# Kernel tuning notes

Measured on AMD Instinct MI355X. Metric: run time of the kernel, lower is better.

Reference implementation:

```python
import jax, jax.numpy as jnp
import numpy as np

DIM = 256
N_CHANNELS = 8
NEIGHBORS = 16


def setup_inputs() -> dict:
    key = jax.random.key(0)
    kx, kw = jax.random.split(key)
    B, N, D = 4, 1024, DIM
    x = jax.random.normal(kx, (B, N, D), dtype=jnp.float32)
    # nn.Linear(dim, dim*2*n_channels, bias=False); store as [in, out] so y = x @ W
    W_qk = jax.random.normal(kw, (D, 2 * N_CHANNELS * D), dtype=jnp.float32) * (D ** -0.5)
    return {"x": x, "W_qk": W_qk}


def _norm_edge(edge):
    # edge: [B, C, N, N]
    norm_row = edge / (edge.sum(axis=-1, keepdims=True) + 1e-6)
    norm_col = norm_row / (norm_row.sum(axis=-2, keepdims=True) + 1e-6)
    # norm_row @ norm_col^T
    return jnp.einsum('bcnk,bcmk->bcnm', norm_row, norm_col)


def reference(x, W_qk):
    B, N, D = x.shape
    C = N_CHANNELS
    scale = D ** -0.5
    qk = (x @ W_qk).reshape(B, N, 2, C, D)
    q = jnp.transpose(qk[:, :, 0], (0, 2, 1, 3))  # [B, C, N, D]
    k = jnp.transpose(qk[:, :, 1], (0, 2, 1, 3))  # [B, C, N, D]
    attn = jax.nn.softmax(jnp.einsum('bcnd,bcmd->bcnm', q, k) * scale, axis=-1)

    # clip(): top-k neighbor mask from channel-summed (detached) attention
    sum_edge = jax.lax.stop_gradient(attn).sum(axis=1)  # [B, N, N]
    kk = min(NEIGHBORS, N)
    _, top_idx = jax.lax.top_k(sum_edge, kk)  # [B, N, kk]
    b_idx = jnp.arange(B)[:, None, None]
    r_idx = jnp.arange(N)[None, :, None]
    mask = jnp.zeros((B, N, N), dtype=attn.dtype).at[b_idx, r_idx, top_idx].set(1.0)
    mask = jnp.maximum(mask, jnp.eye(N, dtype=attn.dtype))  # identity diag
    edge = mask[:, None] * attn  # [B, C, N, N]
    return _norm_edge(edge)
```

## Files before the change

kernel.cpp:

```cpp
#include <hip/hip_runtime.h>
#include <hip/hip_bf16.h>
#include <math.h>

#define BB 4
#define NN 1024
#define DD 256
#define CC 8
#define KNBR 16
#define MAXSEL 17
#define ZCAP (NN * MAXSEL)

typedef _Float16 f16x8_t __attribute__((ext_vector_type(8)));
typedef _Float16 f16x4_t __attribute__((ext_vector_type(4)));
typedef float    f32x4_t __attribute__((ext_vector_type(4)));

__device__ __forceinline__ void gl2lds16(const _Float16* g, _Float16* ldsbase) {
    __builtin_amdgcn_global_load_lds(
        (const __attribute__((address_space(1))) unsigned int*)g,
        (__attribute__((address_space(3))) unsigned int*)ldsbase, 16, 0, 0);
}

__device__ __forceinline__ void split2(float v, _Float16& h, _Float16& l) {
    h = (_Float16)v;
    l = (_Float16)(v - (float)h);
}

__global__ __launch_bounds__(256) void split_all(const float* __restrict__ x,
                                                 const float* __restrict__ W,
                                                 _Float16* __restrict__ xh,
                                                 _Float16* __restrict__ xl,
                                                 _Float16* __restrict__ Wth,
                                                 _Float16* __restrict__ Wtl,
                                                 int* __restrict__ countb) {
    const int tid = threadIdx.x;
    if (blockIdx.x < 1024) {
        int i = (blockIdx.x * 256 + tid) * 4;
        float4 v = *(const float4*)(x + i);
        f16x4_t hv, lv;
        _Float16 h, l;
        split2(v.x, h, l); hv[0] = h; lv[0] = l;
        split2(v.y, h, l); hv[1] = h; lv[1] = l;
        split2(v.z, h, l); hv[2] = h; lv[2] = l;
        split2(v.w, h, l); hv[3] = h; lv[3] = l;
        *(f16x4_t*)(xh + i) = hv;
        *(f16x4_t*)(xl + i) = lv;
    } else {
        const int b2 = blockIdx.x - 1024;
        if (b2 == 0) {
            int4 zz = make_int4(0, 0, 0, 0);
#pragma unroll
            for (int g = 0; g < 4; g++) ((int4*)countb)[tid + 256 * g] = zz;
        }
        __shared__ float t[64][65];
        const int n0 = (b2 & 63) * 64;
        const int k0 = (b2 >> 6) * 64;
#pragma unroll
        for (int i = 0; i < 16; i++) {
            int k = i * 4 + (tid >> 6);
            int n = tid & 63;
            t[k][n] = W[(size_t)(k0 + k) * 4096 + n0 + n];
        }
        __syncthreads();
#pragma unroll
        for (int i = 0; i < 16; i++) {
            int n = i * 4 + (tid >> 6);
            int k = tid & 63;
            _Float16 h, l;
            split2(t[k][n] * 16.f, h, l);
            size_t o = (size_t)(n0 + n) * 256 + k0 + k;
            Wth[o] = h; Wtl[o] = l;
        }
    }
}

#define STG(dst, src, rowbase, kk)                                             \
    do {                                                                       \
        gl2lds16((src) + (size_t)((rowbase) + r_st) * 256 + (kk) + c8,         \
                 &(dst)[(w * 64) * 8]);                                        \
        gl2lds16((src) + (size_t)((rowbase) + 64 + r_st) * 256 + (kk) + c8,    \
                 &(dst)[(256 + w * 64) * 8]);                                  \
    } while (0)

#define MFMA3(accv, AH, AL, BH, BL)                                            \
    do {                                                                       \
        accv = __builtin_amdgcn_mfma_f32_16x16x32_f16(AL, BH, accv, 0, 0, 0);  \
        accv = __builtin_amdgcn_mfma_f32_16x16x32_f16(AH, BL, accv, 0, 0, 0);  \
        accv = __builtin_amdgcn_mfma_f32_16x16x32_f16(AH, BH, accv, 0, 0, 0);  \
    } while (0)

#define COMPUTE(AH, AL, BH, BL)                                                \
    do {                                                                       \
        f16x8_t ah[4], al[4];                                                  \
        _Pragma("unroll")                                                      \
        for (int mi = 0; mi < 4; mi++) {                                       \
            int r = (wr * 64 + mi * 16 + lm) * 32 + qx8;                       \
            ah[mi] = *(const f16x8_t*)&(AH)[r];                                \
            al[mi] = *(const f16x8_t*)&(AL)[r];                                \
        }                                                                      \
        _Pragma("unroll")                                                      \
        for (int ni = 0; ni < 4; ni++) {                                       \
            int rb = (wc * 64 + ni * 16 + lm) * 32 + qx8;                      \
            f16x8_t bh = *(const f16x8_t*)&(BH)[rb];                           \
            f16x8_t bl = *(const f16x8_t*)&(BL)[rb];                           \
            _Pragma("unroll")                                                  \
            for (int mi = 0; mi < 4; mi++)                                     \
                MFMA3(acc[mi][ni], ah[mi], al[mi], bh, bl);                    \
        }                                                                      \
    } while (0)

__global__ __launch_bounds__(256) void gemm_xw_mfma(
        const _Float16* __restrict__ xh, const _Float16* __restrict__ xl,
        const _Float16* __restrict__ wth, const _Float16* __restrict__ wtl,
        _Float16* __restrict__ qh, _Float16* __restrict__ ql,
        _Float16* __restrict__ kh, _Float16* __restrict__ kl) {
    __shared__ __align__(16) char smem[65536];
    _Float16* Ah0 = (_Float16*)smem;
    _Float16* Al0 = (_Float16*)(smem + 8192);
    _Float16* Bh0 = (_Float16*)(smem + 16384);
    _Float16* Bl0 = (_Float16*)(smem + 24576);
    _Float16* Ah1 = (_Float16*)(smem + 32768);
    _Float16* Al1 = (_Float16*)(smem + 40960);
    _Float16* Bh1 = (_Float16*)(smem + 49152);
    _Float16* Bl1 = (_Float16*)(smem + 57344);
    const int tid = threadIdx.x, lane = tid & 63, w = tid >> 6;
    const int wr = w >> 1, wc = w & 1;
    const int lm = lane & 15, quad = lane >> 4;
    const int row0 = blockIdx.y * 128, col0 = blockIdx.x * 128;
    const int r_st = tid >> 2;
    const int c8 = (((tid & 3) ^ ((tid >> 3) & 3)) * 8);
    const int qx8 = ((quad ^ ((lm >> 1) & 3)) * 8);

    f32x4_t acc[4][4];
#pragma unroll
    for (int i = 0; i < 4; i++)
#pragma unroll
        for (int j = 0; j < 4; j++) acc[i][j] = (f32x4_t)(0.f);

    STG(Ah0, xh, row0, 0); STG(Al0, xl, row0, 0);
    STG(Bh0, wth, col0, 0); STG(Bl0, wtl, col0, 0);
    __syncthreads();
#pragma unroll
    for (int t = 0; t < 8; t += 2) {
        {
            int kn = (t + 1) * 32;
            if (t + 1 < 8) {
                STG(Ah1, xh, row0, kn); STG(Al1, xl, row0, kn);
                STG(Bh1, wth, col0, kn); STG(Bl1, wtl, col0, kn);
            }
            COMPUTE(Ah0, Al0, Bh0, Bl0);
            __syncthreads();
        }
        {
            int kn = (t + 2) * 32;
            if (t + 2 < 8) {
                STG(Ah0, xh, row0, kn); STG(Al0, xl, row0, kn);
                STG(Bh0, wth, col0, kn); STG(Bl0, wtl, col0, kn);
            }
            COMPUTE(Ah1, Al1, Bh1, Bl1);
            __syncthreads();
        }
    }

    float* tr = (float*)smem;
    const int s = col0 >> 11, c = (col0 >> 8) & 7, dbase = col0 & 255;
    _Float16* dh = s ? kh : qh;
    _Float16* dl = s ? kl : ql;
    const int rl = tid >> 2;
    const int cb = (tid & 3) * 8;
#pragma unroll
    for (int p = 0; p < 2; p++) {
        if (p) __syncthreads();
        if (wr == p) {
#pragma unroll
            for (int mi = 0; mi < 4; mi++) {
                int rloc = mi * 16 + quad * 4;
#pragma unroll
                for (int ni = 0; ni < 4; ni++) {
                    int cl = wc * 64 + ni * 16 + lm;
#pragma unroll
                    for (int r = 0; r < 4; r++)
                        tr[(rloc + r) * 132 + cl] = acc[mi][ni][r];
                }
            }
        }
        __syncthreads();
        int rr = row0 + p * 64 + rl;
        int bb = rr >> 10, n = rr & 1023;
        size_t base = (((size_t)(bb * CC + c)) * NN + n) * DD + dbase;
#pragma unroll
        for (int g = 0; g < 4; g++) {
            int ccol = g * 32 + cb;
            f16x8_t hv, lv;
#pragma unroll
            for (int e = 0; e < 8; e++) {
                float vv = tr[rl * 132 + ccol + e];
                _Float16 h, l;
                split2(vv, h, l);
                hv[e] = h; lv[e] = l;
            }
            *(f16x8_t*)(dh + base + ccol) = hv;
            *(f16x8_t*)(dl + base + ccol) = lv;
        }
    }
}

__global__ __launch_bounds__(256) void gemm_qkt_mfma(
        const _Float16* __restrict__ qh, const _Float16* __restrict__ ql,
        const _Float16* __restrict__ kh, const _Float16* __restrict__ kl,
        float* __restrict__ attn) {
    __shared__ __align__(16) char smem[65536];
    _Float16* Ah0 = (_Float16*)smem;
    _Float16* Al0 = (_Float16*)(smem + 8192);
    _Float16* Bh0 = (_Float16*)(smem + 16384);
    _Float16* Bl0 = (_Float16*)(smem + 24576);
    _Float16* Ah1 = (_Float16*)(smem + 32768);
    _Float16* Al1 = (_Float16*)(smem + 40960);
    _Float16* Bh1 = (_Float16*)(smem + 49152);
    _Float16* Bl1 = (_Float16*)(smem + 57344);
    const int tid = threadIdx.x, lane = tid & 63, w = tid >> 6;
    const int wr = w >> 1, wc = w & 1;
    const int lm = lane & 15, quad = lane >> 4;
    const int id = blockIdx.x;
    const int rb8 = id & 7, qq = id >> 3;
    const int j = qq & 63, zhi = qq >> 6;
    const int z = zhi * 8 + rb8;
    const int row0 = (j >> 3) * 128, col0 = (j & 7) * 128;
    const size_t zo = (size_t)z * NN * DD;
    float* Cm = attn + (size_t)z * NN * NN;
    const int r_st = tid >> 2;
    const int c8 = (((tid & 3) ^ ((tid >> 3) & 3)) * 8);
    const int qx8 = ((quad ^ ((lm >> 1) & 3)) * 8);
    const float scale = 0.0625f / 256.0f;

    f32x4_t acc[4][4];
#pragma unroll
    for (int i = 0; i < 4; i++)
#pragma unroll
        for (int j2 = 0; j2 < 4; j2++) acc[i][j2] = (f32x4_t)(0.f);

    const _Float16* qhz = qh + zo;
    const _Float16* qlz = ql + zo;
    const _Float16* khz = kh + zo;
    const _Float16* klz = kl + zo;

    STG(Ah0, qhz, row0, 0); STG(Al0, qlz, row0, 0);
    STG(Bh0, khz, col0, 0); STG(Bl0, klz, col0, 0);
    __syncthreads();
#pragma unroll
    for (int t = 0; t < 8; t += 2) {
        {
            int kn = (t + 1) * 32;
            if (t + 1 < 8) {
                STG(Ah1, qhz, row0, kn); STG(Al1, qlz, row0, kn);
                STG(Bh1, khz, col0, kn); STG(Bl1, klz, col0, kn);
            }
            COMPUTE(Ah0, Al0, Bh0, Bl0);
            __syncthreads();
        }
        {
            int kn = (t + 2) * 32;
            if (t + 2 < 8) {
                STG(Ah0, qhz, row0, kn); STG(Al0, qlz, row0, kn);
                STG(Bh0, khz, col0, kn); STG(Bl0, klz, col0, kn);
            }
            COMPUTE(Ah1, Al1, Bh1, Bl1);
            __syncthreads();
        }
    }

#pragma unroll
    for (int mi = 0; mi < 4; mi++)
#pragma unroll
        for (int ni = 0; ni < 4; ni++) {
            int row = row0 + wr * 64 + mi * 16 + quad * 4;
            int col = col0 + wc * 64 + ni * 16 + lm;
#pragma unroll
            for (int r = 0; r < 4; r++)
                Cm[(size_t)(row + r) * NN + col] = acc[mi][ni][r] * scale;
        }
}

__global__ __launch_bounds__(256) void softmax_topk(const float* __restrict__ attn,
                                                    float2* __restrict__ ml,
                                                    int* __restrict__ idx,
                                                    int* __restrict__ cnt,
                                                    int* __restrict__ countb,
                                                    float* __restrict__ colsum) {
    __shared__ float psum[4][1280];
    __shared__ int fsel[MAXSEL];
    __shared__ int fcnt;
    const int bn = blockIdx.x, b = bn >> 10, n = bn & 1023;
    const int tid = threadIdx.x, lane = tid & 63, w = tid >> 6;

    if (tid < CC) colsum[(size_t)(b * CC + tid) * NN + n] = 0.f;

    const int colb = lane * 16;
    const int pb   = lane * 20;
    float4 u[2][4];
#pragma unroll
    for (int p = 0; p < 2; p++) {
        const int c = w * 2 + p;
        const float* rowp = attn + (((size_t)(b * CC + c) * NN + n) * NN) + colb;
#pragma unroll
        for (int g = 0; g < 4; g++) u[p][g] = *(const float4*)(rowp + g * 4);
    }

    float acc[16];
#pragma unroll
    for (int e = 0; e < 16; e++) acc[e] = 0.f;

#pragma unroll
    for (int p = 0; p < 2; p++) {
        const int c = w * 2 + p;
        const float* f = (const float*)&u[p][0];
        float mx = f[0];
#pragma unroll
        for (int e = 1; e < 16; e++) mx = fmaxf(mx, f[e]);
#pragma unroll
        for (int off = 1; off < 64; off <<= 1) mx = fmaxf(mx, __shfl_xor(mx, off));
        float sm = 0.f;
        float pe[16];
#pragma unroll
        for (int e = 0; e < 16; e++) { pe[e] = expf(f[e] - mx); sm += pe[e]; }
#pragma unroll
        for (int off = 1; off < 64; off <<= 1) sm += __shfl_xor(sm, off);
        if (lane == 0) ml[(size_t)(b * CC + c) * NN + n] = make_float2(mx, sm);
        float inv = 1.0f / sm;
#pragma unroll
        for (int e = 0; e < 16; e++) acc[e] += pe[e] * inv;
    }
#pragma unroll
    for (int g = 0; g < 4; g++)
        *(float4*)&psum[w][pb + g * 4] =
            make_float4(acc[g * 4], acc[g * 4 + 1], acc[g * 4 + 2], acc[g * 4 + 3]);
    __syncthreads();

    const int p4 = tid * 4 + (tid >> 2) * 4;
    float4 a0 = *(const float4*)&psum[0][p4];
    float4 a1 = *(const float4*)&psum[1][p4];
    float4 a2 = *(const float4*)&psum[2][p4];
    float4 a3 = *(const float4*)&psum[3][p4];
    float4 vs;
    vs.x = a0.x + a1.x + a2.x + a3.x;
    vs.y = a0.y + a1.y + a2.y + a3.y;
    vs.z = a0.z + a1.z + a2.z + a3.z;
    vs.w = a0.w + a1.w + a2.w + a3.w;
    *(float4*)&psum[0][p4] = vs;
    __syncthreads();

    if (w == 0) {
        unsigned vb[16];
#pragma unroll
        for (int g = 0; g < 4; g++) {
            float4 t4 = *(const float4*)&psum[0][pb + g * 4];
            vb[g * 4 + 0] = __float_as_uint(t4.x);
            vb[g * 4 + 1] = __float_as_uint(t4.y);
            vb[g * 4 + 2] = __float_as_uint(t4.z);
            vb[g * 4 + 3] = __float_as_uint(t4.w);
        }
        unsigned lo = 0u, hi = 0x7F800000u;
        while (lo < hi) {
            unsigned mid = lo + ((hi - lo) >> 1);
            int c = 0;
#pragma unroll
            for (int e = 0; e < 16; e++)
                c += (int)__popcll(__ballot(vb[e] > mid));
            if (c <= 15) hi = mid; else lo = mid + 1;
        }
        const unsigned V = hi;
        int cgt = 0, ceq = 0;
#pragma unroll
        for (int e = 0; e < 16; e++) {
            cgt += (vb[e] > V) ? 1 : 0;
            ceq += (vb[e] == V) ? 1 : 0;
        }
        int pk = cgt | (ceq << 16);
        int incl = pk;
#pragma unroll
        for (int o = 1; o < 64; o <<= 1) {
            int v2 = __shfl_up(incl, o);
            if (lane >= o) incl += v2;
        }
        int tot = __shfl(incl, 63);
        int c1 = tot & 0xffff;
        int need = KNBR - c1;
        int excl = incl - pk;
        int pg = excl & 0xffff;
        int pe2 = excl >> 16;
        int lg = 0, le = 0;
#pragma unroll
        for (int e = 0; e < 16; e++) {
            if (vb[e] > V) {
                fsel[pg + lg] = colb + e; lg++;
            } else if (vb[e] == V) {
                if (pe2 + le < need) fsel[c1 + pe2 + le] = colb + e;
                le++;
            }
        }
        if (lane == 0) {
            bool has = false;
#pragma unroll
            for (int t2 = 0; t2 < KNBR; t2++)
                if (fsel[t2] == n) has = true;
            int c = KNBR;
            if (!has) { fsel[KNBR] = n; c = KNBR + 1; }
            fcnt = c;
            cnt[bn] = c;
        }
    }
    __syncthreads();
    if (tid < fcnt) {
        idx[bn * MAXSEL + tid] = fsel[tid];
        atomicAdd(&countb[b * NN + fsel[tid]], 1);
    }
}

__global__ __launch_bounds__(256) void scan_offb(const int* __restrict__ countb,
                                                 int* __restrict__ offb,
                                                 int* __restrict__ curs) {
    __shared__ int wtot[4];
    const int b = blockIdx.x, tid = threadIdx.x, lane = tid & 63, w = tid >> 6;
    int c0 = countb[b * NN + tid * 4 + 0];
    int c1 = countb[b * NN + tid * 4 + 1];
    int c2 = countb[b * NN + tid * 4 + 2];
    int c3 = countb[b * NN + tid * 4 + 3];
    int tsum = c0 + c1 + c2 + c3;
    int incl = tsum;
#pragma unroll
    for (int off = 1; off < 64; off <<= 1) {
        int v = __shfl_up(incl, off);
        if (lane >= off) incl += v;
    }
    if (lane == 63) wtot[w] = incl;
    __syncthreads();
    int woff = 0;
    for (int i = 0; i < w; i++) woff += wtot[i];
    int base = woff + incl - tsum;
    int o0 = base, o1 = base + c0, o2 = base + c0 + c1, o3 = base + c0 + c1 + c2;
    offb[b * NN + tid * 4 + 0] = o0;
    offb[b * NN + tid * 4 + 1] = o1;
    offb[b * NN + tid * 4 + 2] = o2;
    offb[b * NN + tid * 4 + 3] = o3;
#pragma unroll
    for (int c = 0; c < CC; c++) {
        int z = b * CC + c;
        curs[z * NN + tid * 4 + 0] = o0;
        curs[z * NN + tid * 4 + 1] = o1;
        curs[z * NN + tid * 4 + 2] = o2;
        curs[z * NN + tid * 4 + 3] = o3;
    }
}

__global__ __launch_bounds__(256) void rownorm_fill(const float* __restrict__ attn,
                                                    const float2* __restrict__ ml,
                                                    const int* __restrict__ idx,
                                                    const int* __restrict__ cnt,
                                                    int* __restrict__ curs,
                                                    float* __restrict__ nr,
                                                    float* __restrict__ colsum,
                                                    int2* __restrict__ epack) {
    const int t = blockIdx.x * 256 + threadIdx.x;
    const int z = t >> 10, n = t & 1023;
    const int b = z >> 3;
    const int bn = b * NN + n;
    const int c_ = cnt[bn];
    const float* arow = attn + (size_t)t * NN;
    const float2 MM = ml[t];
    const float invl = 1.0f / MM.y;
    const size_t zb = (size_t)z * ZCAP;
    float a[MAXSEL];
    int kk[MAXSEL];
    float s = 0.f;
#pragma unroll
    for (int j = 0; j < MAXSEL; j++) {
        if (j < c_) {
            kk[j] = idx[bn * MAXSEL + j];
            float p = expf(arow[kk[j]] - MM.x) * invl;
            a[j] = p; s += p;
        }
    }
    const float inv = 1.f / (s + 1e-6f);
#pragma unroll
    for (int j = 0; j < MAXSEL; j++) {
        if (j < c_) {
            float v = a[j] * inv;
            nr[(size_t)t * MAXSEL + j] = v;
            atomicAdd(&colsum[(size_t)z * NN + kk[j]], v);
            int p = atomicAdd(&curs[z * NN + kk[j]], 1);
            epack[zb + p] = make_int2(n, __float_as_int(v));
        }
    }
}

__global__ __launch_bounds__(256) void out_sparse(const float* __restrict__ nr,
                                                  const int* __restrict__ idx,
                                                  const int* __restrict__ cnt,
                                                  const int* __restrict__ offb,
                                                  const int* __restrict__ countb,
                                                  const float* __restrict__ colsum,
                                                  const int2* __restrict__ epack,
                                                  float* __restrict__ out) {
    __shared__ float row[4][NN];
    const int tid = threadIdx.x, lane = tid & 63, w = tid >> 6;
    const int t = blockIdx.x * 4 + w;
    const int z = t >> 10;
    const int b = z >> 3;
    const int bn = b * NN + (t & 1023);
    const size_t zb = (size_t)z * ZCAP;

    f32x4_t zz = (f32x4_t)(0.f);
#pragma unroll
    for (int q = 0; q < 4; q++) ((f32x4_t*)row[w])[q * 64 + lane] = zz;

    const int c_ = cnt[bn];
    float sc = 0.f;
    int off = 0, len = 0;
    if (lane < c_) {
        int k = idx[bn * MAXSEL + lane];
        float wgt = nr[(size_t)t * MAXSEL + lane];
        sc = wgt / (colsum[(size_t)z * NN + k] + 1e-6f);
        off = offb[b * NN + k];
        len = countb[b * NN + k];
    }

    const int half = lane >> 5, l0 = lane & 31;
    for (int j = half; j < c_; j += 2) {
        float scj = __shfl(sc, j);
        int offj = __shfl(off, j);
        int lenj = __shfl(len, j);
        for (int l = l0; l < lenj; l += 32) {
            int2 ev = epack[zb + offj + l];
            atomicAdd(&row[w][ev.x], scj * __int_as_float(ev.y));
        }
    }
    const size_t ob = (size_t)t * NN;
    f32x4_t* op = (f32x4_t*)(out + ob);
#pragma unroll
    for (int q = 0; q < 4; q++)
        op[q * 64 + lane] = ((f32x4_t*)row[w])[q * 64 + lane];
}

extern "C" void kernel_launch(void* const* d_in, const int* in_sizes, int n_in,
                              void* d_out, int out_size, void* d_ws, size_t ws_size,
                              hipStream_t stream) {
    const float* x = (const float*)d_in[0];
    const float* W = (const float*)d_in[1];
    float* out = (float*)d_out;
    char* ws = (char*)d_ws;

    float* attn = (float*)d_out;

    _Float16* qh  = (_Float16*)(ws);
    _Float16* ql  = (_Float16*)(ws + 16777216ull);
    _Float16* kh  = (_Float16*)(ws + 33554432ull);
    _Float16* kl  = (_Float16*)(ws + 50331648ull);
    _Float16* xh  = (_Float16*)(ws + 67108864ull);
    _Float16* xl  = (_Float16*)(ws + 69206016ull);
    _Float16* wth = (_Float16*)(ws + 71303168ull);
    _Float16* wtl = (_Float16*)(ws + 73400320ull);
    int*    idx  = (int*)   (ws + 75497472ull);
    int*    cnt  = (int*)   (ws + 75776000ull);
    float*  nr   = (float*) (ws + 75792384ull);
    float*  colsum = (float*)(ws + 78020608ull);
    float2* ml   = (float2*)(ws + 78151680ull);
    int*    countb = (int*) (ws + 78413824ull);
    int*    offb = (int*)   (ws + 78430208ull);
    int*    curs = (int*)   (ws + 78446592ull);
    int2*   epack = (int2*) (ws + 78577664ull);

    split_all<<<1280, 256, 0, stream>>>(x, W, xh, xl, wth, wtl, countb);
    gemm_xw_mfma<<<dim3(32, 32), 256, 0, stream>>>(xh, xl, wth, wtl,
                                                   qh, ql, kh, kl);
    gemm_qkt_mfma<<<2048, 256, 0, stream>>>(qh, ql, kh, kl, attn);
    softmax_topk<<<4096, 256, 0, stream>>>(attn, ml, idx, cnt, countb, colsum);
    scan_offb<<<4, 256, 0, stream>>>(countb, offb, curs);
    rownorm_fill<<<128, 256, 0, stream>>>(attn, ml, idx, cnt, curs, nr, colsum,
                                          epack);
    out_sparse<<<8192, 256, 0, stream>>>(nr, idx, cnt, offb, countb, colsum,
                                         epack, out);
}
```

Measured before the change: 394.8 us.

## Share edge bucket positions across channels and process all channels per row block

Bucket positions for the sparse column-normalised product are now computed once per batch in the scan kernel, with a per-edge position map, instead of separately per channel with atomics in rownorm_fill. Edge values are stored channel-interleaved (8 floats per edge), so one out_sparse block handles all 8 channels of a row. That block reads each edge index once and issues vector loads for the values. This cuts duplicated index traffic and cursor atomics, but scan_offb now does the serial atomic fill with only 4 blocks, and out_sparse uses 32KB of LDS per block, which may lower occupancy.

```diff
diff --git a/kernel.cpp b/kernel.cpp
--- a/kernel.cpp
+++ b/kernel.cpp
@@ -417,7 +417,11 @@
 
 __global__ __launch_bounds__(256) void scan_offb(const int* __restrict__ countb,
                                                  int* __restrict__ offb,
-                                                 int* __restrict__ curs) {
+                                                 int* __restrict__ curs,
+                                                 const int* __restrict__ cnt,
+                                                 const int* __restrict__ idx,
+                                                 int* __restrict__ eidx,
+                                                 int* __restrict__ pmap) {
     __shared__ int wtot[4];
     const int b = blockIdx.x, tid = threadIdx.x, lane = tid & 63, w = tid >> 6;
     int c0 = countb[b * NN + tid * 4 + 0];
@@ -441,13 +445,27 @@
     offb[b * NN + tid * 4 + 1] = o1;
     offb[b * NN + tid * 4 + 2] = o2;
     offb[b * NN + tid * 4 + 3] = o3;
-#pragma unroll
-    for (int c = 0; c < CC; c++) {
-        int z = b * CC + c;
-        curs[z * NN + tid * 4 + 0] = o0;
-        curs[z * NN + tid * 4 + 1] = o1;
-        curs[z * NN + tid * 4 + 2] = o2;
-        curs[z * NN + tid * 4 + 3] = o3;
+    curs[b * NN + tid * 4 + 0] = o0;
+    curs[b * NN + tid * 4 + 1] = o1;
+    curs[b * NN + tid * 4 + 2] = o2;
+    curs[b * NN + tid * 4 + 3] = o3;
+    __syncthreads();
+
+    for (int r = 0; r < 4; r++) {
+        int n = tid + r * 256;
+        int bn = b * NN + n;
+        int c_ = cnt[bn];
+        int start = n & 15;
+        for (int jj = 0; jj < MAXSEL; jj++) {
+            if (jj < c_) {
+                int j = jj + start;
+                if (j >= c_) j -= c_;
+                int k = idx[bn * MAXSEL + j];
+                int p = atomicAdd(&curs[b * NN + k], 1);
+                eidx[b * ZCAP + p] = n;
+                pmap[bn * MAXSEL + j] = p;
+            }
+        }
     }
 }
 
@@ -455,19 +473,18 @@
                                                     const float2* __restrict__ ml,
                                                     const int* __restrict__ idx,
                                                     const int* __restrict__ cnt,
-                                                    int* __restrict__ curs,
+                                                    const int* __restrict__ pmap,
                                                     float* __restrict__ nr,
                                                     float* __restrict__ colsum,
-                                                    int2* __restrict__ epack) {
+                                                    float* __restrict__ eval8) {
     const int t = blockIdx.x * 256 + threadIdx.x;
     const int z = t >> 10, n = t & 1023;
-    const int b = z >> 3;
+    const int b = z >> 3, c = z & 7;
     const int bn = b * NN + n;
     const int c_ = cnt[bn];
     const float* arow = attn + (size_t)t * NN;
     const float2 MM = ml[t];
     const float invl = 1.0f / MM.y;
-    const size_t zb = (size_t)z * ZCAP;
     float a[MAXSEL];
     int kk[MAXSEL];
     float s = 0.f;
@@ -486,58 +503,86 @@
             float v = a[j] * inv;
             nr[(size_t)t * MAXSEL + j] = v;
             atomicAdd(&colsum[(size_t)z * NN + kk[j]], v);
-            int p = atomicAdd(&curs[z * NN + kk[j]], 1);
-            epack[zb + p] = make_int2(n, __float_as_int(v));
-        }
-    }
-}
-
-__global__ __launch_bounds__(256) void out_sparse(const float* __restrict__ nr,
+            int p = pmap[bn * MAXSEL + j];
+            eval8[((size_t)b * ZCAP + p) * 8 + c] = v;
+        }
+    }
+}
+
+__global__ __launch_bounds__(512) void out_sparse(const float* __restrict__ nr,
                                                   const int* __restrict__ idx,
                                                   const int* __restrict__ cnt,
                                                   const int* __restrict__ offb,
                                                   const int* __restrict__ countb,
                                                   const float* __restrict__ colsum,
-                                                  const int2* __restrict__ epack,
+                                                  const int* __restrict__ eidx,
+                                                  const float* __restrict__ eval8,
                                                   float* __restrict__ out) {
-    __shared__ float row[4][NN];
+    __shared__ float acc[CC][NN];
+    __shared__ float scm[CC][MAXSEL];
+    __shared__ int goffs[MAXSEL];
+    __shared__ int glens[MAXSEL];
+    const int bn = blockIdx.x;
+    const int b = bn >> 10, n = bn & 1023;
     const int tid = threadIdx.x, lane = tid & 63, w = tid >> 6;
-    const int t = blockIdx.x * 4 + w;
-    const int z = t >> 10;
-    const int b = z >> 3;
-    const int bn = b * NN + (t & 1023);
-    const size_t zb = (size_t)z * ZCAP;
+    const int c_ = cnt[bn];
 
     f32x4_t zz = (f32x4_t)(0.f);
 #pragma unroll
-    for (int q = 0; q < 4; q++) ((f32x4_t*)row[w])[q * 64 + lane] = zz;
-
-    const int c_ = cnt[bn];
-    float sc = 0.f;
-    int off = 0, len = 0;
-    if (lane < c_) {
-        int k = idx[bn * MAXSEL + lane];
-        float wgt = nr[(size_t)t * MAXSEL + lane];
-        sc = wgt / (colsum[(size_t)z * NN + k] + 1e-6f);
-        off = offb[b * NN + k];
-        len = countb[b * NN + k];
-    }
-
-    const int half = lane >> 5, l0 = lane & 31;
-    for (int j = half; j < c_; j += 2) {
-        float scj = __shfl(sc, j);
-        int offj = __shfl(off, j);
-        int lenj = __shfl(len, j);
-        for (int l = l0; l < lenj; l += 32) {
-            int2 ev = epack[zb + offj + l];
-            atomicAdd(&row[w][ev.x], scj * __int_as_float(ev.y));
-        }
-    }
-    const size_t ob = (size_t)t * NN;
-    f32x4_t* op = (f32x4_t*)(out + ob);
-#pragma unroll
-    for (int q = 0; q < 4; q++)
-        op[q * 64 + lane] = ((f32x4_t*)row[w])[q * 64 + lane];
+    for (int q = 0; q < 4; q++) ((f32x4_t*)acc)[tid + q * 512] = zz;
+
+    if (tid < 256) {
+        int c = tid >> 5, j = tid & 31;
+        if (j < MAXSEL) {
+            float sc = 0.f;
+            if (j < c_) {
+                int z = b * CC + c;
+                int k = idx[bn * MAXSEL + j];
+                float wgt = nr[((size_t)z * NN + n) * MAXSEL + j];
+                sc = wgt / (colsum[(size_t)z * NN + k] + 1e-6f);
+            }
+            scm[c][j] = sc;
+        }
+    } else if (tid < 256 + MAXSEL) {
+        int j = tid - 256;
+        int off = 0, len = 0;
+        if (j < c_) {
+            int k = idx[bn * MAXSEL + j];
+            off = offb[b * NN + k];
+            len = countb[b * NN + k];
+        }
+        goffs[j] = off; glens[j] = len;
+    }
+    __syncthreads();
+
+    for (int j = w; j < c_; j += 8) {
+        const int off = goffs[j], len = glens[j];
+        const float s0 = scm[0][j], s1 = scm[1][j], s2 = scm[2][j], s3 = scm[3][j];
+        const float s4 = scm[4][j], s5 = scm[5][j], s6 = scm[6][j], s7 = scm[7][j];
+        for (int l = lane; l < len; l += 64) {
+            int m = eidx[b * ZCAP + off + l];
+            const float* vp = eval8 + ((size_t)b * ZCAP + off + l) * 8;
+            f32x4_t va = *(const f32x4_t*)vp;
+            f32x4_t vb2 = *(const f32x4_t*)(vp + 4);
+            atomicAdd(&acc[0][m], s0 * va[0]);
+            atomicAdd(&acc[1][m], s1 * va[1]);
+            atomicAdd(&acc[2][m], s2 * va[2]);
+            atomicAdd(&acc[3][m], s3 * va[3]);
+            atomicAdd(&acc[4][m], s4 * vb2[0]);
+            atomicAdd(&acc[5][m], s5 * vb2[1]);
+            atomicAdd(&acc[6][m], s6 * vb2[2]);
+            atomicAdd(&acc[7][m], s7 * vb2[3]);
+        }
+    }
+    __syncthreads();
+
+#pragma unroll
+    for (int q = 0; q < 4; q++) {
+        int i4 = tid + q * 512;
+        int c = i4 >> 8, m4 = i4 & 255;
+        *(f32x4_t*)(out + ((size_t)(b * CC + c) * NN + n) * NN + m4 * 4) =
+            ((f32x4_t*)acc)[i4];
+    }
 }
 
 extern "C" void kernel_launch(void* const* d_in, const int* in_sizes, int n_in,
@@ -566,16 +611,18 @@
     int*    countb = (int*) (ws + 78413824ull);
     int*    offb = (int*)   (ws + 78430208ull);
     int*    curs = (int*)   (ws + 78446592ull);
-    int2*   epack = (int2*) (ws + 78577664ull);
+    int*    eidx = (int*)   (ws + 78577664ull);
+    float*  eval8 = (float*)(ws + 78856192ull);
+    int*    pmap = (int*)   (ws + 81084416ull);
 
     split_all<<<1280, 256, 0, stream>>>(x, W, xh, xl, wth, wtl, countb);
     gemm_xw_mfma<<<dim3(32, 32), 256, 0, stream>>>(xh, xl, wth, wtl,
                                                    qh, ql, kh, kl);
     gemm_qkt_mfma<<<2048, 256, 0, stream>>>(qh, ql, kh, kl, attn);
     softmax_topk<<<4096, 256, 0, stream>>>(attn, ml, idx, cnt, countb, colsum);
-    scan_offb<<<4, 256, 0, stream>>>(countb, offb, curs);
-    rownorm_fill<<<128, 256, 0, stream>>>(attn, ml, idx, cnt, curs, nr, colsum,
-                                          epack);
-    out_sparse<<<8192, 256, 0, stream>>>(nr, idx, cnt, offb, countb, colsum,
-                                         epack, out);
-}
+    scan_offb<<<4, 256, 0, stream>>>(countb, offb, curs, cnt, idx, eidx, pmap);
+    rownorm_fill<<<128, 256, 0, stream>>>(attn, ml, idx, cnt, pmap, nr, colsum,
+                                          eval8);
+    out_sparse<<<4096, 512, 0, stream>>>(nr, idx, cnt, offb, countb, colsum,
+                                         eidx, eval8, out);
+}
```

After: 415.2 us. +5.2%, slower.
